# Kernel tuning notes

Hardware: AMD Instinct MI355X
Metric: run time of the kernel (lower is better)

Reference implementation:

```python
import jax, jax.numpy as jnp
import numpy as np

N_GRAPHS = 2048  # number of molecules in the DGL batch


def gcn_layer(h, src, dst, W, residual, n_nodes):
    # DGL sum aggregation: scatter-add neighbor features to dst, then linear + relu
    agg = jax.ops.segment_sum(h[src], dst, num_segments=n_nodes)  # [N, d_in]
    out = jax.nn.relu(agg @ W)  # [N, d_out]
    if residual:
        out = out + h
    return out


def setup_inputs() -> dict:
    key = jax.random.key(0)
    ks = jax.random.split(key, 12)
    N, E, D_N = 100000, 400000, 35
    x = jax.random.normal(ks[0], (N, D_N), dtype=jnp.float32)
    edge_src = jax.random.randint(ks[1], (E,), 0, N)
    edge_dst = jax.random.randint(ks[2], (E,), 0, N)
    graph_ids = jnp.sort(jax.random.randint(ks[3], (N,), 0, N_GRAPHS))
    W_emb = jax.random.normal(ks[4], (D_N, 8), dtype=jnp.float32) * 0.1
    W_g0 = jax.random.normal(ks[5], (8, 128), dtype=jnp.float32) * 0.1
    W_g1 = jax.random.normal(ks[6], (128, 128), dtype=jnp.float32) * 0.05
    W_g2 = jax.random.normal(ks[7], (128, 128), dtype=jnp.float32) * 0.05
    W_p1 = jax.random.normal(ks[8], (128, 64), dtype=jnp.float32) * 0.05
    W_p2 = jax.random.normal(ks[9], (64, 1), dtype=jnp.float32) * 0.05
    b_p2 = jnp.zeros((1,), dtype=jnp.float32)
    return dict(x=x, W_emb=W_emb, W_g0=W_g0, W_g1=W_g1, W_g2=W_g2,
                W_p1=W_p1, W_p2=W_p2, b_p2=b_p2,
                edge_src=edge_src, edge_dst=edge_dst, graph_ids=graph_ids)


def reference(x, W_emb, W_g0, W_g1, W_g2, W_p1, W_p2, b_p2,
              edge_src, edge_dst, graph_ids):
    n = x.shape[0]
    # GCNEmbed: initial node embedding (d_n -> 8, no bias)
    h = x @ W_emb
    # GCN layers: sum aggregation; first layer no residual, rest residual
    h = gcn_layer(h, edge_src, edge_dst, W_g0, False, n)  # 8 -> 128
    h = gcn_layer(h, edge_src, edge_dst, W_g1, True, n)   # 128 -> 128
    h = gcn_layer(h, edge_src, edge_dst, W_g2, True, n)   # 128 -> 128
    # SumPooling over each graph in the batch
    g_emb = jax.ops.segment_sum(h, graph_ids, num_segments=N_GRAPHS)  # [G, 128]
    # pred head: Linear(128,64,no bias) -> ReLU -> Linear(64,1,bias)
    pred = jax.nn.relu(g_emb @ W_p1) @ W_p2 + b_p2  # [G, 1]
    return pred
```

## Files before the change

### kernel.cpp

```cpp
#include <hip/hip_runtime.h>


constexpr int NUM_GRAPHS = 2048;

typedef _Float16 f16x8 __attribute__((ext_vector_type(8)));
typedef float f32x4 __attribute__((ext_vector_type(4)));

__global__ __launch_bounds__(256) void k_embed(const float* __restrict__ x,
                                               const float* __restrict__ Wemb,
                                               float* __restrict__ h0, int N) {
  __shared__ float sx[32 * 35];
  __shared__ float sw[35 * 8];
  int n0 = blockIdx.x * 32;
  int cnt = min(32, N - n0);
  int nf = cnt * 35;
  for (int i = threadIdx.x; i < nf; i += 256) sx[i] = x[(size_t)n0 * 35 + i];
  for (int i = threadIdx.x; i < 35 * 8; i += 256) sw[i] = Wemb[i];
  __syncthreads();
  int nl = threadIdx.x >> 3;
  int c = threadIdx.x & 7;
  if (nl < cnt) {
    float acc = 0.f;
#pragma unroll
    for (int k = 0; k < 35; ++k) acc = fmaf(sx[nl * 35 + k], sw[k * 8 + c], acc);
    h0[(size_t)(n0 + nl) * 8 + c] = acc;
  }
}

__global__ __launch_bounds__(256) void k_hist(const int* __restrict__ dst,
                                              int* counts, int E) {
  int e = blockIdx.x * 256 + threadIdx.x;
  if (e < E) atomicAdd(&counts[dst[e]], 1);
}

__global__ __launch_bounds__(256) void k_scan1(const int* __restrict__ counts,
                                               int* __restrict__ offs,
                                               int* __restrict__ partials, int N) {
  __shared__ int s[256];
  int i = blockIdx.x * 256 + threadIdx.x;
  int v = (i < N) ? counts[i] : 0;
  s[threadIdx.x] = v;
  __syncthreads();
#pragma unroll
  for (int d = 1; d < 256; d <<= 1) {
    int t = (threadIdx.x >= d) ? s[threadIdx.x - d] : 0;
    __syncthreads();
    s[threadIdx.x] += t;
    __syncthreads();
  }
  if (i < N) offs[i] = s[threadIdx.x] - v;
  if (threadIdx.x == 255) partials[blockIdx.x] = s[255];
}

__global__ __launch_bounds__(512) void k_scan2(int* partials, int nb) {
  __shared__ int s[512];
  int t = threadIdx.x;
  int orig = (t < nb) ? partials[t] : 0;
  s[t] = orig;
  __syncthreads();
#pragma unroll
  for (int d = 1; d < 512; d <<= 1) {
    int v = (t >= d) ? s[t - d] : 0;
    __syncthreads();
    s[t] += v;
    __syncthreads();
  }
  if (t < nb) partials[t] = s[t] - orig;
}

__global__ __launch_bounds__(256) void k_scan3(int* __restrict__ offs,
                                               const int* __restrict__ partials,
                                               int* __restrict__ cursor, int N) {
  int i = blockIdx.x * 256 + threadIdx.x;
  if (i < N) {
    int v = offs[i] + partials[blockIdx.x];
    offs[i] = v;
    cursor[i] = v;
  }
}

__global__ __launch_bounds__(256) void k_fill(const int* __restrict__ src,
                                              const int* __restrict__ dst,
                                              int* cursor, int* __restrict__ csr,
                                              int E) {
  int e = blockIdx.x * 256 + threadIdx.x;
  if (e < E) {
    int slot = atomicAdd(&cursor[dst[e]], 1);
    csr[slot] = src[e];
  }
}

__global__ __launch_bounds__(128) void k_prepw(const float* __restrict__ W1,
                                               const float* __restrict__ W2,
                                               _Float16* __restrict__ WT1,
                                               _Float16* __restrict__ WT2) {
  int n = blockIdx.x & 127;
  const float* W = (blockIdx.x < 128) ? W1 : W2;
  _Float16* WT = (blockIdx.x < 128) ? WT1 : WT2;
  int k = threadIdx.x;
  WT[(size_t)n * 128 + k] = (_Float16)W[(size_t)k * 128 + n];
}

__global__ __launch_bounds__(256, 4) void k_layer0(const float* __restrict__ h0,
                                                   const int* __restrict__ csr,
                                                   const int* __restrict__ offs,
                                                   const int* __restrict__ cnts,
                                                   const float* __restrict__ W,
                                                   _Float16* __restrict__ out,
                                                   int N, int E) {
  __shared__ int sidx0[6144];
  __shared__ float sw[8 * 128];
  for (int i = threadIdx.x; i < 1024; i += 256) sw[i] = W[i];
  int n0 = blockIdx.x * 256;
  int e0 = offs[n0];
  int e1 = (n0 + 256 < N) ? offs[n0 + 256] : E;
  int nedge = e1 - e0;
  bool staged = (nedge <= 6144);
  if (staged) {
    for (int i = threadIdx.x; i < nedge; i += 256) sidx0[i] = csr[e0 + i];
  }
  __syncthreads();

  int n = n0 + (int)threadIdx.x;
  float4 A0 = {0.f, 0.f, 0.f, 0.f}, A1 = {0.f, 0.f, 0.f, 0.f};
  int cnt = (n < N) ? cnts[n] : 0;
  int sb = (n < N) ? (offs[n] - e0) : 0;
  if (staged) {
    for (int e = 0; e < cnt; e += 4) {
      int i0 = sidx0[sb + e];
      int i1 = sidx0[sb + min(e + 1, cnt - 1)];
      int i2 = sidx0[sb + min(e + 2, cnt - 1)];
      int i3 = sidx0[sb + min(e + 3, cnt - 1)];
      float s1 = (e + 1 < cnt) ? 1.f : 0.f;
      float s2 = (e + 2 < cnt) ? 1.f : 0.f;
      float s3 = (e + 3 < cnt) ? 1.f : 0.f;
      const float4* p0 = reinterpret_cast<const float4*>(h0 + (size_t)i0 * 8);
      const float4* p1 = reinterpret_cast<const float4*>(h0 + (size_t)i1 * 8);
      const float4* p2 = reinterpret_cast<const float4*>(h0 + (size_t)i2 * 8);
      const float4* p3 = reinterpret_cast<const float4*>(h0 + (size_t)i3 * 8);
      float4 a0 = p0[0], a1 = p0[1];
      float4 b0 = p1[0], b1 = p1[1];
      float4 c0 = p2[0], c1 = p2[1];
      float4 d0 = p3[0], d1 = p3[1];
      __builtin_amdgcn_sched_barrier(0);
      A0.x += a0.x; A0.y += a0.y; A0.z += a0.z; A0.w += a0.w;
      A1.x += a1.x; A1.y += a1.y; A1.z += a1.z; A1.w += a1.w;
      A0.x = fmaf(s1, b0.x, A0.x); A0.y = fmaf(s1, b0.y, A0.y);
      A0.z = fmaf(s1, b0.z, A0.z); A0.w = fmaf(s1, b0.w, A0.w);
      A1.x = fmaf(s1, b1.x, A1.x); A1.y = fmaf(s1, b1.y, A1.y);
      A1.z = fmaf(s1, b1.z, A1.z); A1.w = fmaf(s1, b1.w, A1.w);
      A0.x = fmaf(s2, c0.x, A0.x); A0.y = fmaf(s2, c0.y, A0.y);
      A0.z = fmaf(s2, c0.z, A0.z); A0.w = fmaf(s2, c0.w, A0.w);
      A1.x = fmaf(s2, c1.x, A1.x); A1.y = fmaf(s2, c1.y, A1.y);
      A1.z = fmaf(s2, c1.z, A1.z); A1.w = fmaf(s2, c1.w, A1.w);
      A0.x = fmaf(s3, d0.x, A0.x); A0.y = fmaf(s3, d0.y, A0.y);
      A0.z = fmaf(s3, d0.z, A0.z); A0.w = fmaf(s3, d0.w, A0.w);
      A1.x = fmaf(s3, d1.x, A1.x); A1.y = fmaf(s3, d1.y, A1.y);
      A1.z = fmaf(s3, d1.z, A1.z); A1.w = fmaf(s3, d1.w, A1.w);
    }
  } else {
    for (int e = 0; e < cnt; ++e) {
      int i0 = csr[offs[n] + e];
      const float4* p0 = reinterpret_cast<const float4*>(h0 + (size_t)i0 * 8);
      float4 a0 = p0[0], a1 = p0[1];
      A0.x += a0.x; A0.y += a0.y; A0.z += a0.z; A0.w += a0.w;
      A1.x += a1.x; A1.y += a1.y; A1.z += a1.z; A1.w += a1.w;
    }
  }
  if (n >= N) return;

  float a[8] = {A0.x, A0.y, A0.z, A0.w, A1.x, A1.y, A1.z, A1.w};
  size_t base = (size_t)n * 128;
#pragma unroll
  for (int c0 = 0; c0 < 128; c0 += 32) {
    float o[32];
#pragma unroll
    for (int j = 0; j < 32; ++j) o[j] = 0.f;
#pragma unroll
    for (int k = 0; k < 8; ++k) {
      float av = a[k];
      const float* swk = &sw[k * 128 + c0];
#pragma unroll
      for (int j = 0; j < 32; ++j) o[j] = fmaf(av, swk[j], o[j]);
    }
#pragma unroll
    for (int v = 0; v < 4; ++v) {
      f16x8 st;
#pragma unroll
      for (int i = 0; i < 8; ++i) st[i] = (_Float16)fmaxf(o[v * 8 + i], 0.f);
      *reinterpret_cast<f16x8*>(out + base + c0 + v * 8) = st;
    }
  }
}

__device__ __forceinline__ void acc_f16x8(float4& a0, float4& a1, const f16x8 h) {
  a0.x += (float)h[0]; a0.y += (float)h[1]; a0.z += (float)h[2]; a0.w += (float)h[3];
  a1.x += (float)h[4]; a1.y += (float)h[5]; a1.z += (float)h[6]; a1.w += (float)h[7];
}
__device__ __forceinline__ void acc_fma8(float4& a0, float4& a1, const f16x8 h,
                                         float s) {
  a0.x = fmaf(s, (float)h[0], a0.x); a0.y = fmaf(s, (float)h[1], a0.y);
  a0.z = fmaf(s, (float)h[2], a0.z); a0.w = fmaf(s, (float)h[3], a0.w);
  a1.x = fmaf(s, (float)h[4], a1.x); a1.y = fmaf(s, (float)h[5], a1.y);
  a1.z = fmaf(s, (float)h[6], a1.z); a1.w = fmaf(s, (float)h[7], a1.w);
}

__global__ __launch_bounds__(256, 4) void k_gcn_fused(
    const _Float16* __restrict__ H, const int* __restrict__ csr,
    const int* __restrict__ offs, const int* __restrict__ cnts,
    const _Float16* __restrict__ WT, _Float16* __restrict__ out,
    float* G, const int* __restrict__ gid, int N, int E, int mode) {
  __shared__ _Float16 sa_h[64 * 136];
  int* sidx = reinterpret_cast<int*>(sa_h);
  int n0 = blockIdx.x * 64;

  int e0 = offs[n0];
  int e1 = (n0 + 64 < N) ? offs[n0 + 64] : E;
  int nedge = e1 - e0;
  bool staged = (nedge <= 64 * 136 / 2);

  if (staged) {
    for (int i = threadIdx.x; i < nedge; i += 256) sidx[i] = csr[e0 + i];
  }
  __syncthreads();

  int q = threadIdx.x >> 6;
  int l = threadIdx.x & 63;
  {
    int n = n0 + l;
    float4 acc[8];
#pragma unroll
    for (int i = 0; i < 8; ++i) acc[i] = make_float4(0.f, 0.f, 0.f, 0.f);
    int cnt = (n < N) ? cnts[n] : 0;
    int sb = (n < N) ? (offs[n] - e0) : 0;
    const _Float16* Hq = H + q * 32;
    if (staged) {
      for (int e = 0; e < cnt; e += 4) {
        int i0 = sidx[sb + e];
        int i1 = sidx[sb + min(e + 1, cnt - 1)];
        int i2 = sidx[sb + min(e + 2, cnt - 1)];
        int i3 = sidx[sb + min(e + 3, cnt - 1)];
        float s1 = (e + 1 < cnt) ? 1.f : 0.f;
        float s2 = (e + 2 < cnt) ? 1.f : 0.f;
        float s3 = (e + 3 < cnt) ? 1.f : 0.f;
        const f16x8* r0 = reinterpret_cast<const f16x8*>(Hq + (size_t)i0 * 128);
        const f16x8* r1 = reinterpret_cast<const f16x8*>(Hq + (size_t)i1 * 128);
        const f16x8* r2 = reinterpret_cast<const f16x8*>(Hq + (size_t)i2 * 128);
        const f16x8* r3 = reinterpret_cast<const f16x8*>(Hq + (size_t)i3 * 128);
        f16x8 a0 = r0[0], a1 = r0[1], a2 = r0[2], a3 = r0[3];
        f16x8 b0 = r1[0], b1 = r1[1], b2 = r1[2], b3 = r1[3];
        f16x8 c0 = r2[0], c1 = r2[1], c2 = r2[2], c3 = r2[3];
        f16x8 d0 = r3[0], d1 = r3[1], d2 = r3[2], d3 = r3[3];
        __builtin_amdgcn_sched_barrier(0);
        acc_f16x8(acc[0], acc[1], a0); acc_f16x8(acc[2], acc[3], a1);
        acc_f16x8(acc[4], acc[5], a2); acc_f16x8(acc[6], acc[7], a3);
        acc_fma8(acc[0], acc[1], b0, s1); acc_fma8(acc[2], acc[3], b1, s1);
        acc_fma8(acc[4], acc[5], b2, s1); acc_fma8(acc[6], acc[7], b3, s1);
        acc_fma8(acc[0], acc[1], c0, s2); acc_fma8(acc[2], acc[3], c1, s2);
        acc_fma8(acc[4], acc[5], c2, s2); acc_fma8(acc[6], acc[7], c3, s2);
        acc_fma8(acc[0], acc[1], d0, s3); acc_fma8(acc[2], acc[3], d1, s3);
        acc_fma8(acc[4], acc[5], d2, s3); acc_fma8(acc[6], acc[7], d3, s3);
      }
    } else {
      int s = (n < N) ? offs[n] : 0;
      for (int e = 0; e < cnt; ++e) {
        int s0 = csr[s + e];
        const f16x8* r0 = reinterpret_cast<const f16x8*>(Hq + (size_t)s0 * 128);
        f16x8 a0 = r0[0], a1 = r0[1], a2 = r0[2], a3 = r0[3];
        acc_f16x8(acc[0], acc[1], a0); acc_f16x8(acc[2], acc[3], a1);
        acc_f16x8(acc[4], acc[5], a2); acc_f16x8(acc[6], acc[7], a3);
      }
    }
    __syncthreads();
    float* af = reinterpret_cast<float*>(acc);
#pragma unroll
    for (int j = 0; j < 4; ++j) {
      f16x8 st;
#pragma unroll
      for (int i = 0; i < 8; ++i) st[i] = (_Float16)af[j * 8 + i];
      *reinterpret_cast<f16x8*>(&sa_h[l * 136 + q * 32 + j * 8]) = st;
    }
  }
  __syncthreads();

  {
    int w = threadIdx.x >> 6;
    int lane = threadIdx.x & 63;
    int lr = lane & 15;
    int lg = lane >> 4;
    f32x4 C[4][2];
#pragma unroll
    for (int mt = 0; mt < 4; ++mt)
#pragma unroll
      for (int nt = 0; nt < 2; ++nt) C[mt][nt] = (f32x4){0.f, 0.f, 0.f, 0.f};
    const _Float16* WTb = WT + (size_t)(w * 32) * 128;
#pragma unroll
    for (int kk = 0; kk < 4; ++kk) {
      int k0 = kk * 32 + lg * 8;
      f16x8 a0 = *reinterpret_cast<const f16x8*>(&sa_h[(0 + lr) * 136 + k0]);
      f16x8 a1 = *reinterpret_cast<const f16x8*>(&sa_h[(16 + lr) * 136 + k0]);
      f16x8 a2 = *reinterpret_cast<const f16x8*>(&sa_h[(32 + lr) * 136 + k0]);
      f16x8 a3 = *reinterpret_cast<const f16x8*>(&sa_h[(48 + lr) * 136 + k0]);
      f16x8 b0 = *reinterpret_cast<const f16x8*>(&WTb[(size_t)lr * 128 + k0]);
      f16x8 b1 = *reinterpret_cast<const f16x8*>(&WTb[(size_t)(16 + lr) * 128 + k0]);
      C[0][0] = __builtin_amdgcn_mfma_f32_16x16x32_f16(a0, b0, C[0][0], 0, 0, 0);
      C[1][0] = __builtin_amdgcn_mfma_f32_16x16x32_f16(a1, b0, C[1][0], 0, 0, 0);
      C[2][0] = __builtin_amdgcn_mfma_f32_16x16x32_f16(a2, b0, C[2][0], 0, 0, 0);
      C[3][0] = __builtin_amdgcn_mfma_f32_16x16x32_f16(a3, b0, C[3][0], 0, 0, 0);
      C[0][1] = __builtin_amdgcn_mfma_f32_16x16x32_f16(a0, b1, C[0][1], 0, 0, 0);
      C[1][1] = __builtin_amdgcn_mfma_f32_16x16x32_f16(a1, b1, C[1][1], 0, 0, 0);
      C[2][1] = __builtin_amdgcn_mfma_f32_16x16x32_f16(a2, b1, C[2][1], 0, 0, 0);
      C[3][1] = __builtin_amdgcn_mfma_f32_16x16x32_f16(a3, b1, C[3][1], 0, 0, 0);
    }
    __syncthreads();
#pragma unroll
    for (int mt = 0; mt < 4; ++mt)
#pragma unroll
      for (int nt = 0; nt < 2; ++nt)
#pragma unroll
        for (int r = 0; r < 4; ++r) {
          int row = mt * 16 + lg * 4 + r;
          int col = w * 32 + nt * 16 + lr;
          sa_h[row * 136 + col] = (_Float16)fmaxf(C[mt][nt][r], 0.f);
        }
  }
  __syncthreads();

  int nl = threadIdx.x >> 4;
  int j0 = (threadIdx.x & 15) * 8;
  if (mode == 0) {
#pragma unroll
    for (int r = 0; r < 4; ++r) {
      int row = nl + 16 * r;
      int n = n0 + row;
      if (n < N) {
        size_t base = (size_t)n * 128 + j0;
        f16x8 vv = *reinterpret_cast<const f16x8*>(&sa_h[row * 136 + j0]);
        f16x8 hh = *reinterpret_cast<const f16x8*>(H + base);
        f16x8 o;
#pragma unroll
        for (int i = 0; i < 8; ++i) o[i] = (_Float16)((float)vv[i] + (float)hh[i]);
        *reinterpret_cast<f16x8*>(out + base) = o;
      }
    }
  } else {
#pragma unroll
    for (int r = 0; r < 4; ++r) {
      int row = nl + 16 * r;
      int n = n0 + row;
      if (n < N) {
        size_t base = (size_t)n * 128 + j0;
        f16x8 vv = *reinterpret_cast<const f16x8*>(&sa_h[row * 136 + j0]);
        f16x8 hh = *reinterpret_cast<const f16x8*>(H + base);
        f16x8 o;
#pragma unroll
        for (int i = 0; i < 8; ++i) o[i] = (_Float16)((float)vv[i] + (float)hh[i]);
        *reinterpret_cast<f16x8*>(&sa_h[row * 136 + j0]) = o;
      }
    }
    __syncthreads();
    int grp = threadIdx.x >> 7;
    int j = threadIdx.x & 127;
    int r0 = grp * 32;
    int nfirst = n0 + r0;
    if (nfirst < N) {
      float pacc = 0.f;
      int cur = gid[nfirst];
      for (int r = r0; r < r0 + 32; ++r) {
        int n = n0 + r;
        if (n >= N) break;
        int g2 = gid[n];
        if (g2 != cur) {
          atomicAdd(&G[(size_t)cur * 128 + j], pacc);
          pacc = 0.f;
          cur = g2;
        }
        pacc += (float)sa_h[r * 136 + j];
      }
      atomicAdd(&G[(size_t)cur * 128 + j], pacc);
    }
  }
}

__global__ __launch_bounds__(64) void k_head(const float* __restrict__ g,
                                             const float* __restrict__ W1,
                                             const float* __restrict__ W2,
                                             const float* __restrict__ b,
                                             float* __restrict__ out) {
  int gi = blockIdx.x;
  int j = threadIdx.x;
  __shared__ float sg[128];
  sg[j] = g[(size_t)gi * 128 + j];
  sg[j + 64] = g[(size_t)gi * 128 + 64 + j];
  __syncthreads();
  float acc = 0.f;
#pragma unroll
  for (int k = 0; k < 128; ++k) acc = fmaf(sg[k], W1[k * 64 + j], acc);
  acc = fmaxf(acc, 0.f) * W2[j];
#pragma unroll
  for (int off = 32; off > 0; off >>= 1) acc += __shfl_down(acc, off);
  if (j == 0) out[gi] = acc + b[0];
}

extern "C" void kernel_launch(void* const* d_in, const int* in_sizes, int n_in,
                              void* d_out, int out_size, void* d_ws, size_t ws_size,
                              hipStream_t stream) {
  const float* x    = (const float*)d_in[0];
  const float* Wemb = (const float*)d_in[1];
  const float* Wg0  = (const float*)d_in[2];
  const float* Wg1  = (const float*)d_in[3];
  const float* Wg2  = (const float*)d_in[4];
  const float* Wp1  = (const float*)d_in[5];
  const float* Wp2  = (const float*)d_in[6];
  const float* bp2  = (const float*)d_in[7];
  const int* esrc   = (const int*)d_in[8];
  const int* edst   = (const int*)d_in[9];
  const int* gids   = (const int*)d_in[10];
  int N = in_sizes[0] / 35;
  int E = in_sizes[8];
  float* out = (float*)d_out;

  char* wp = (char*)d_ws;
  float* h0 = (float*)wp;            wp += (size_t)N * 8 * sizeof(float);
  _Float16* P = (_Float16*)wp;       wp += (size_t)N * 128 * sizeof(_Float16);
  _Float16* Q = (_Float16*)wp;       wp += (size_t)N * 128 * sizeof(_Float16);
  float* G  = (float*)wp;            wp += (size_t)NUM_GRAPHS * 128 * sizeof(float);
  int* counts   = (int*)wp;          wp += (size_t)N * sizeof(int);
  int* offs     = (int*)wp;          wp += (size_t)N * sizeof(int);
  int* cursor   = (int*)wp;          wp += (size_t)N * sizeof(int);
  int* partials = (int*)wp;          wp += 512 * sizeof(int);
  int* csr      = (int*)wp;          wp += (size_t)E * sizeof(int);
  _Float16* WT1 = (_Float16*)wp;     wp += (size_t)128 * 128 * sizeof(_Float16);
  _Float16* WT2 = (_Float16*)wp;

  int nbE = (E + 255) / 256;
  int nbN = (N + 255) / 256;

  k_embed<<<(N + 31) / 32, 256, 0, stream>>>(x, Wemb, h0, N);
  k_prepw<<<256, 128, 0, stream>>>(Wg1, Wg2, WT1, WT2);

  hipMemsetAsync(counts, 0, (size_t)N * sizeof(int), stream);
  k_hist<<<nbE, 256, 0, stream>>>(edst, counts, E);
  k_scan1<<<nbN, 256, 0, stream>>>(counts, offs, partials, N);
  k_scan2<<<1, 512, 0, stream>>>(partials, nbN);
  k_scan3<<<nbN, 256, 0, stream>>>(offs, partials, cursor, N);
  k_fill<<<nbE, 256, 0, stream>>>(esrc, edst, cursor, csr, E);

  hipMemsetAsync(G, 0, (size_t)NUM_GRAPHS * 128 * sizeof(float), stream);

  k_layer0<<<(N + 255) / 256, 256, 0, stream>>>(h0, csr, offs, counts, Wg0, P,
                                                N, E);

  k_gcn_fused<<<(N + 63) / 64, 256, 0, stream>>>(P, csr, offs, counts, WT1, Q,
                                                 nullptr, nullptr, N, E, 0);

  k_gcn_fused<<<(N + 63) / 64, 256, 0, stream>>>(Q, csr, offs, counts, WT2, nullptr,
                                                 G, gids, N, E, 1);

  k_head<<<NUM_GRAPHS, 64, 0, stream>>>(G, Wp1, Wp2, bp2, out);
}
```

Before: 172.7 us.

## Merge prep kernels, fuse scan stages, store embedding in fp16, simplify gather loops

Embedding, degree histogram, weight transpose and pooled-buffer zeroing now run as one multi-role launch, and the second and third scan stages are merged so each block rescans the partial sums itself. This removes several kernel launches and a memset. The layer-0 input embedding is stored as fp16, halving gather traffic at some precision cost. The gather loops switch from masked clamped loads to a main loop plus remainder, with a second accumulator in layer 0 and the sched_barrier removed; the layer-0 staging buffer is halved, so more blocks may take the unstaged fallback path.

```diff
diff --git a/kernel.cpp b/kernel.cpp
--- a/kernel.cpp
+++ b/kernel.cpp
@@ -6,31 +6,60 @@
 typedef _Float16 f16x8 __attribute__((ext_vector_type(8)));
 typedef float f32x4 __attribute__((ext_vector_type(4)));
 
-__global__ __launch_bounds__(256) void k_embed(const float* __restrict__ x,
-                                               const float* __restrict__ Wemb,
-                                               float* __restrict__ h0, int N) {
-  __shared__ float sx[32 * 35];
-  __shared__ float sw[35 * 8];
-  int n0 = blockIdx.x * 32;
-  int cnt = min(32, N - n0);
-  int nf = cnt * 35;
-  for (int i = threadIdx.x; i < nf; i += 256) sx[i] = x[(size_t)n0 * 35 + i];
-  for (int i = threadIdx.x; i < 35 * 8; i += 256) sw[i] = Wemb[i];
-  __syncthreads();
-  int nl = threadIdx.x >> 3;
-  int c = threadIdx.x & 7;
-  if (nl < cnt) {
-    float acc = 0.f;
-#pragma unroll
-    for (int k = 0; k < 35; ++k) acc = fmaf(sx[nl * 35 + k], sw[k * 8 + c], acc);
-    h0[(size_t)(n0 + nl) * 8 + c] = acc;
-  }
-}
-
-__global__ __launch_bounds__(256) void k_hist(const int* __restrict__ dst,
-                                              int* counts, int E) {
-  int e = blockIdx.x * 256 + threadIdx.x;
-  if (e < E) atomicAdd(&counts[dst[e]], 1);
+__device__ __forceinline__ void acc_f16x8(float4& a0, float4& a1, const f16x8 h) {
+  a0.x += (float)h[0]; a0.y += (float)h[1]; a0.z += (float)h[2]; a0.w += (float)h[3];
+  a1.x += (float)h[4]; a1.y += (float)h[5]; a1.z += (float)h[6]; a1.w += (float)h[7];
+}
+
+__global__ __launch_bounds__(256) void k_prep(
+    const float* __restrict__ x, const float* __restrict__ Wemb,
+    _Float16* __restrict__ h0, const int* __restrict__ edst, int* counts,
+    const float* __restrict__ W1, const float* __restrict__ W2,
+    _Float16* __restrict__ WT1, _Float16* __restrict__ WT2,
+    float* __restrict__ G, int N, int E, int embedB, int histB) {
+  int b = blockIdx.x;
+  if (b < embedB) {
+    __shared__ float sx[32 * 35];
+    __shared__ float sw[35 * 8];
+    int n0 = b * 32;
+    int cnt = min(32, N - n0);
+    int nf = cnt * 35;
+    for (int i = threadIdx.x; i < nf; i += 256) sx[i] = x[(size_t)n0 * 35 + i];
+    for (int i = threadIdx.x; i < 35 * 8; i += 256) sw[i] = Wemb[i];
+    __syncthreads();
+    int nl = threadIdx.x >> 3;
+    int c = threadIdx.x & 7;
+    if (nl < cnt) {
+      float acc = 0.f;
+#pragma unroll
+      for (int k = 0; k < 35; ++k)
+        acc = fmaf(sx[nl * 35 + k], sw[k * 8 + c], acc);
+      h0[(size_t)(n0 + nl) * 8 + c] = (_Float16)acc;
+    }
+    return;
+  }
+  b -= embedB;
+  if (b < histB) {
+    int e = b * 256 + threadIdx.x;
+    if (e < E) atomicAdd(&counts[edst[e]], 1);
+    return;
+  }
+  b -= histB;
+  if (b < 128) {
+    int k = threadIdx.x & 127;
+    if (threadIdx.x < 128)
+      WT1[(size_t)b * 128 + k] = (_Float16)W1[(size_t)k * 128 + b];
+    else
+      WT2[(size_t)b * 128 + k] = (_Float16)W2[(size_t)k * 128 + b];
+    return;
+  }
+  b -= 128;
+  if (b < 64) {
+    float4* g4 = reinterpret_cast<float4*>(G);
+#pragma unroll
+    for (int r = 0; r < 4; ++r)
+      g4[b * 1024 + r * 256 + threadIdx.x] = make_float4(0.f, 0.f, 0.f, 0.f);
+  }
 }
 
 __global__ __launch_bounds__(256) void k_scan1(const int* __restrict__ counts,
@@ -52,30 +81,32 @@
   if (threadIdx.x == 255) partials[blockIdx.x] = s[255];
 }
 
-__global__ __launch_bounds__(512) void k_scan2(int* partials, int nb) {
+__global__ __launch_bounds__(512) void k_scan23(int* __restrict__ offs,
+                                                const int* __restrict__ partials,
+                                                int* __restrict__ cursor,
+                                                int N, int nb) {
   __shared__ int s[512];
+  __shared__ int base;
   int t = threadIdx.x;
-  int orig = (t < nb) ? partials[t] : 0;
-  s[t] = orig;
+  int v = (t < nb) ? partials[t] : 0;
+  s[t] = v;
   __syncthreads();
 #pragma unroll
   for (int d = 1; d < 512; d <<= 1) {
-    int v = (t >= d) ? s[t - d] : 0;
-    __syncthreads();
-    s[t] += v;
-    __syncthreads();
-  }
-  if (t < nb) partials[t] = s[t] - orig;
-}
-
-__global__ __launch_bounds__(256) void k_scan3(int* __restrict__ offs,
-                                               const int* __restrict__ partials,
-                                               int* __restrict__ cursor, int N) {
-  int i = blockIdx.x * 256 + threadIdx.x;
-  if (i < N) {
-    int v = offs[i] + partials[blockIdx.x];
-    offs[i] = v;
-    cursor[i] = v;
+    int u = (t >= d) ? s[t - d] : 0;
+    __syncthreads();
+    s[t] += u;
+    __syncthreads();
+  }
+  if (t == (int)blockIdx.x) base = s[t] - v;
+  __syncthreads();
+  if (t < 256) {
+    int i = blockIdx.x * 256 + t;
+    if (i < N) {
+      int val = offs[i] + base;
+      offs[i] = val;
+      cursor[i] = val;
+    }
   }
 }
 
@@ -90,84 +121,60 @@
   }
 }
 
-__global__ __launch_bounds__(128) void k_prepw(const float* __restrict__ W1,
-                                               const float* __restrict__ W2,
-                                               _Float16* __restrict__ WT1,
-                                               _Float16* __restrict__ WT2) {
-  int n = blockIdx.x & 127;
-  const float* W = (blockIdx.x < 128) ? W1 : W2;
-  _Float16* WT = (blockIdx.x < 128) ? WT1 : WT2;
-  int k = threadIdx.x;
-  WT[(size_t)n * 128 + k] = (_Float16)W[(size_t)k * 128 + n];
-}
-
-__global__ __launch_bounds__(256, 4) void k_layer0(const float* __restrict__ h0,
-                                                   const int* __restrict__ csr,
-                                                   const int* __restrict__ offs,
-                                                   const int* __restrict__ cnts,
-                                                   const float* __restrict__ W,
-                                                   _Float16* __restrict__ out,
-                                                   int N, int E) {
-  __shared__ int sidx0[6144];
+__global__ __launch_bounds__(256) void k_layer0(const _Float16* __restrict__ h0,
+                                                const int* __restrict__ csr,
+                                                const int* __restrict__ offs,
+                                                const int* __restrict__ cnts,
+                                                const float* __restrict__ W,
+                                                _Float16* __restrict__ out,
+                                                int N, int E) {
   __shared__ float sw[8 * 128];
+  __shared__ int sidx[3072];
   for (int i = threadIdx.x; i < 1024; i += 256) sw[i] = W[i];
   int n0 = blockIdx.x * 256;
   int e0 = offs[n0];
   int e1 = (n0 + 256 < N) ? offs[n0 + 256] : E;
   int nedge = e1 - e0;
-  bool staged = (nedge <= 6144);
+  bool staged = (nedge <= 3072);
   if (staged) {
-    for (int i = threadIdx.x; i < nedge; i += 256) sidx0[i] = csr[e0 + i];
+    for (int i = threadIdx.x; i < nedge; i += 256) sidx[i] = csr[e0 + i];
   }
   __syncthreads();
 
   int n = n0 + (int)threadIdx.x;
-  float4 A0 = {0.f, 0.f, 0.f, 0.f}, A1 = {0.f, 0.f, 0.f, 0.f};
+  float4 A0 = {0.f, 0.f, 0.f, 0.f}, A1 = A0, B0 = A0, B1 = A0;
   int cnt = (n < N) ? cnts[n] : 0;
   int sb = (n < N) ? (offs[n] - e0) : 0;
   if (staged) {
-    for (int e = 0; e < cnt; e += 4) {
-      int i0 = sidx0[sb + e];
-      int i1 = sidx0[sb + min(e + 1, cnt - 1)];
-      int i2 = sidx0[sb + min(e + 2, cnt - 1)];
-      int i3 = sidx0[sb + min(e + 3, cnt - 1)];
-      float s1 = (e + 1 < cnt) ? 1.f : 0.f;
-      float s2 = (e + 2 < cnt) ? 1.f : 0.f;
-      float s3 = (e + 3 < cnt) ? 1.f : 0.f;
-      const float4* p0 = reinterpret_cast<const float4*>(h0 + (size_t)i0 * 8);
-      const float4* p1 = reinterpret_cast<const float4*>(h0 + (size_t)i1 * 8);
-      const float4* p2 = reinterpret_cast<const float4*>(h0 + (size_t)i2 * 8);
-      const float4* p3 = reinterpret_cast<const float4*>(h0 + (size_t)i3 * 8);
-      float4 a0 = p0[0], a1 = p0[1];
-      float4 b0 = p1[0], b1 = p1[1];
-      float4 c0 = p2[0], c1 = p2[1];
-      float4 d0 = p3[0], d1 = p3[1];
-      __builtin_amdgcn_sched_barrier(0);
-      A0.x += a0.x; A0.y += a0.y; A0.z += a0.z; A0.w += a0.w;
-      A1.x += a1.x; A1.y += a1.y; A1.z += a1.z; A1.w += a1.w;
-      A0.x = fmaf(s1, b0.x, A0.x); A0.y = fmaf(s1, b0.y, A0.y);
-      A0.z = fmaf(s1, b0.z, A0.z); A0.w = fmaf(s1, b0.w, A0.w);
-      A1.x = fmaf(s1, b1.x, A1.x); A1.y = fmaf(s1, b1.y, A1.y);
-      A1.z = fmaf(s1, b1.z, A1.z); A1.w = fmaf(s1, b1.w, A1.w);
-      A0.x = fmaf(s2, c0.x, A0.x); A0.y = fmaf(s2, c0.y, A0.y);
-      A0.z = fmaf(s2, c0.z, A0.z); A0.w = fmaf(s2, c0.w, A0.w);
-      A1.x = fmaf(s2, c1.x, A1.x); A1.y = fmaf(s2, c1.y, A1.y);
-      A1.z = fmaf(s2, c1.z, A1.z); A1.w = fmaf(s2, c1.w, A1.w);
-      A0.x = fmaf(s3, d0.x, A0.x); A0.y = fmaf(s3, d0.y, A0.y);
-      A0.z = fmaf(s3, d0.z, A0.z); A0.w = fmaf(s3, d0.w, A0.w);
-      A1.x = fmaf(s3, d1.x, A1.x); A1.y = fmaf(s3, d1.y, A1.y);
-      A1.z = fmaf(s3, d1.z, A1.z); A1.w = fmaf(s3, d1.w, A1.w);
+    int e = 0;
+    for (; e + 4 <= cnt; e += 4) {
+      int i0 = sidx[sb + e], i1 = sidx[sb + e + 1];
+      int i2 = sidx[sb + e + 2], i3 = sidx[sb + e + 3];
+      f16x8 v0 = *reinterpret_cast<const f16x8*>(h0 + (size_t)i0 * 8);
+      f16x8 v1 = *reinterpret_cast<const f16x8*>(h0 + (size_t)i1 * 8);
+      f16x8 v2 = *reinterpret_cast<const f16x8*>(h0 + (size_t)i2 * 8);
+      f16x8 v3 = *reinterpret_cast<const f16x8*>(h0 + (size_t)i3 * 8);
+      acc_f16x8(A0, A1, v0);
+      acc_f16x8(B0, B1, v1);
+      acc_f16x8(A0, A1, v2);
+      acc_f16x8(B0, B1, v3);
+    }
+    for (; e < cnt; ++e) {
+      int i0 = sidx[sb + e];
+      f16x8 v0 = *reinterpret_cast<const f16x8*>(h0 + (size_t)i0 * 8);
+      acc_f16x8(A0, A1, v0);
     }
   } else {
+    int s = (n < N) ? offs[n] : 0;
     for (int e = 0; e < cnt; ++e) {
-      int i0 = csr[offs[n] + e];
-      const float4* p0 = reinterpret_cast<const float4*>(h0 + (size_t)i0 * 8);
-      float4 a0 = p0[0], a1 = p0[1];
-      A0.x += a0.x; A0.y += a0.y; A0.z += a0.z; A0.w += a0.w;
-      A1.x += a1.x; A1.y += a1.y; A1.z += a1.z; A1.w += a1.w;
+      int i0 = csr[s + e];
+      f16x8 v0 = *reinterpret_cast<const f16x8*>(h0 + (size_t)i0 * 8);
+      acc_f16x8(A0, A1, v0);
     }
   }
   if (n >= N) return;
+  A0.x += B0.x; A0.y += B0.y; A0.z += B0.z; A0.w += B0.w;
+  A1.x += B1.x; A1.y += B1.y; A1.z += B1.z; A1.w += B1.w;
 
   float a[8] = {A0.x, A0.y, A0.z, A0.w, A1.x, A1.y, A1.z, A1.w};
   size_t base = (size_t)n * 128;
@@ -191,18 +198,6 @@
       *reinterpret_cast<f16x8*>(out + base + c0 + v * 8) = st;
     }
   }
-}
-
-__device__ __forceinline__ void acc_f16x8(float4& a0, float4& a1, const f16x8 h) {
-  a0.x += (float)h[0]; a0.y += (float)h[1]; a0.z += (float)h[2]; a0.w += (float)h[3];
-  a1.x += (float)h[4]; a1.y += (float)h[5]; a1.z += (float)h[6]; a1.w += (float)h[7];
-}
-__device__ __forceinline__ void acc_fma8(float4& a0, float4& a1, const f16x8 h,
-                                         float s) {
-  a0.x = fmaf(s, (float)h[0], a0.x); a0.y = fmaf(s, (float)h[1], a0.y);
-  a0.z = fmaf(s, (float)h[2], a0.z); a0.w = fmaf(s, (float)h[3], a0.w);
-  a1.x = fmaf(s, (float)h[4], a1.x); a1.y = fmaf(s, (float)h[5], a1.y);
-  a1.z = fmaf(s, (float)h[6], a1.z); a1.w = fmaf(s, (float)h[7], a1.w);
 }
 
 __global__ __launch_bounds__(256, 4) void k_gcn_fused(
@@ -235,14 +230,10 @@
     int sb = (n < N) ? (offs[n] - e0) : 0;
     const _Float16* Hq = H + q * 32;
     if (staged) {
-      for (int e = 0; e < cnt; e += 4) {
-        int i0 = sidx[sb + e];
-        int i1 = sidx[sb + min(e + 1, cnt - 1)];
-        int i2 = sidx[sb + min(e + 2, cnt - 1)];
-        int i3 = sidx[sb + min(e + 3, cnt - 1)];
-        float s1 = (e + 1 < cnt) ? 1.f : 0.f;
-        float s2 = (e + 2 < cnt) ? 1.f : 0.f;
-        float s3 = (e + 3 < cnt) ? 1.f : 0.f;
+      int e = 0;
+      for (; e + 4 <= cnt; e += 4) {
+        int i0 = sidx[sb + e], i1 = sidx[sb + e + 1];
+        int i2 = sidx[sb + e + 2], i3 = sidx[sb + e + 3];
         const f16x8* r0 = reinterpret_cast<const f16x8*>(Hq + (size_t)i0 * 128);
         const f16x8* r1 = reinterpret_cast<const f16x8*>(Hq + (size_t)i1 * 128);
         const f16x8* r2 = reinterpret_cast<const f16x8*>(Hq + (size_t)i2 * 128);
@@ -251,15 +242,21 @@
         f16x8 b0 = r1[0], b1 = r1[1], b2 = r1[2], b3 = r1[3];
         f16x8 c0 = r2[0], c1 = r2[1], c2 = r2[2], c3 = r2[3];
         f16x8 d0 = r3[0], d1 = r3[1], d2 = r3[2], d3 = r3[3];
-        __builtin_amdgcn_sched_barrier(0);
         acc_f16x8(acc[0], acc[1], a0); acc_f16x8(acc[2], acc[3], a1);
         acc_f16x8(acc[4], acc[5], a2); acc_f16x8(acc[6], acc[7], a3);
-        acc_fma8(acc[0], acc[1], b0, s1); acc_fma8(acc[2], acc[3], b1, s1);
-        acc_fma8(acc[4], acc[5], b2, s1); acc_fma8(acc[6], acc[7], b3, s1);
-        acc_fma8(acc[0], acc[1], c0, s2); acc_fma8(acc[2], acc[3], c1, s2);
-        acc_fma8(acc[4], acc[5], c2, s2); acc_fma8(acc[6], acc[7], c3, s2);
-        acc_fma8(acc[0], acc[1], d0, s3); acc_fma8(acc[2], acc[3], d1, s3);
-        acc_fma8(acc[4], acc[5], d2, s3); acc_fma8(acc[6], acc[7], d3, s3);
+        acc_f16x8(acc[0], acc[1], b0); acc_f16x8(acc[2], acc[3], b1);
+        acc_f16x8(acc[4], acc[5], b2); acc_f16x8(acc[6], acc[7], b3);
+        acc_f16x8(acc[0], acc[1], c0); acc_f16x8(acc[2], acc[3], c1);
+        acc_f16x8(acc[4], acc[5], c2); acc_f16x8(acc[6], acc[7], c3);
+        acc_f16x8(acc[0], acc[1], d0); acc_f16x8(acc[2], acc[3], d1);
+        acc_f16x8(acc[4], acc[5], d2); acc_f16x8(acc[6], acc[7], d3);
+      }
+      for (; e < cnt; ++e) {
+        int s0 = sidx[sb + e];
+        const f16x8* r0 = reinterpret_cast<const f16x8*>(Hq + (size_t)s0 * 128);
+        f16x8 a0 = r0[0], a1 = r0[1], a2 = r0[2], a3 = r0[3];
+        acc_f16x8(acc[0], acc[1], a0); acc_f16x8(acc[2], acc[3], a1);
+        acc_f16x8(acc[4], acc[5], a2); acc_f16x8(acc[6], acc[7], a3);
       }
     } else {
       int s = (n < N) ? offs[n] : 0;
@@ -421,7 +418,7 @@
   float* out = (float*)d_out;
 
   char* wp = (char*)d_ws;
-  float* h0 = (float*)wp;            wp += (size_t)N * 8 * sizeof(float);
+  _Float16* h0 = (_Float16*)wp;      wp += (size_t)N * 8 * sizeof(_Float16);
   _Float16* P = (_Float16*)wp;       wp += (size_t)N * 128 * sizeof(_Float16);
   _Float16* Q = (_Float16*)wp;       wp += (size_t)N * 128 * sizeof(_Float16);
   float* G  = (float*)wp;            wp += (size_t)NUM_GRAPHS * 128 * sizeof(float);
@@ -435,18 +432,16 @@
 
   int nbE = (E + 255) / 256;
   int nbN = (N + 255) / 256;
-
-  k_embed<<<(N + 31) / 32, 256, 0, stream>>>(x, Wemb, h0, N);
-  k_prepw<<<256, 128, 0, stream>>>(Wg1, Wg2, WT1, WT2);
+  int embedB = (N + 31) / 32;
 
   hipMemsetAsync(counts, 0, (size_t)N * sizeof(int), stream);
-  k_hist<<<nbE, 256, 0, stream>>>(edst, counts, E);
+
+  k_prep<<<embedB + nbE + 128 + 64, 256, 0, stream>>>(
+      x, Wemb, h0, edst, counts, Wg1, Wg2, WT1, WT2, G, N, E, embedB, nbE);
+
   k_scan1<<<nbN, 256, 0, stream>>>(counts, offs, partials, N);
-  k_scan2<<<1, 512, 0, stream>>>(partials, nbN);
-  k_scan3<<<nbN, 256, 0, stream>>>(offs, partials, cursor, N);
+  k_scan23<<<nbN, 512, 0, stream>>>(offs, partials, cursor, N, nbN);
   k_fill<<<nbE, 256, 0, stream>>>(esrc, edst, cursor, csr, E);
-
-  hipMemsetAsync(G, 0, (size_t)NUM_GRAPHS * 128 * sizeof(float), stream);
 
   k_layer0<<<(N + 255) / 256, 256, 0, stream>>>(h0, csr, offs, counts, Wg0, P,
                                                 N, E);
```

New measurement: 159.5 us. -7.6%, faster.
